# Performance work log

Hardware: AMD Instinct MI355X
Metric: run time of the kernel (lower is better)

## Reference

```python
import jax, jax.numpy as jnp
import numpy as np

I, H, O = 32, 64, 8  # input_size, hidden_layer, output_size
B, T = 4096, 256


def setup_inputs() -> dict:
    key = jax.random.key(0)
    ks = jax.random.split(key, 7)
    s_ih = 1.0 / np.sqrt(H)
    return {
        "x": jax.random.normal(ks[0], (B, T, I), dtype=jnp.float32),
        # PyTorch nn.LSTM params, gate order [i, f, g, o]
        "W_ih": jax.random.uniform(ks[1], (4 * H, I), jnp.float32, -s_ih, s_ih),
        "W_hh": jax.random.uniform(ks[2], (4 * H, H), jnp.float32, -s_ih, s_ih),
        "b_ih": jax.random.uniform(ks[3], (4 * H,), jnp.float32, -s_ih, s_ih),
        "b_hh": jax.random.uniform(ks[4], (4 * H,), jnp.float32, -s_ih, s_ih),
        "W_fc": jax.random.uniform(ks[5], (O, H), jnp.float32, -s_ih, s_ih),
        "b_fc": jax.random.uniform(ks[6], (O,), jnp.float32, -s_ih, s_ih),
    }


def reference(x, W_ih, W_hh, b_ih, b_hh, W_fc, b_fc):
    # Precompute input-to-hidden projections for all timesteps in one GEMM.
    # [B, T, 4H]
    x_proj = jnp.einsum('bti,gi->btg', x, W_ih) + b_ih + b_hh

    def step(carry, xp_t):
        h, c = carry  # [B, H] each
        gates = xp_t + h @ W_hh.T  # [B, 4H]
        i_g, f_g, g_g, o_g = jnp.split(gates, 4, axis=-1)
        i_g = jax.nn.sigmoid(i_g)
        f_g = jax.nn.sigmoid(f_g)
        g_g = jnp.tanh(g_g)
        o_g = jax.nn.sigmoid(o_g)
        c = f_g * c + i_g * g_g
        h = o_g * jnp.tanh(c)
        return (h, c), None

    h0 = jnp.zeros((x.shape[0], H), dtype=x.dtype)
    c0 = jnp.zeros((x.shape[0], H), dtype=x.dtype)
    # scan over time axis: move T to leading axis
    (h_T, c_T), _ = jax.lax.scan(step, (h0, c0), jnp.swapaxes(x_proj, 0, 1))
    # out[:, -1, :] == final hidden state for single-layer batch_first LSTM
    return h_T @ W_fc.T + b_fc
```

## Files before the change

### kernel.cpp

```cpp
#include <hip/hip_runtime.h>
#include <hip/hip_bf16.h>


#define T_LEN 256
#define I_SZ  32
#define H_SZ  64
#define O_SZ  8
#define BR    8
#define HS    72

typedef __attribute__((ext_vector_type(8))) short short8;
typedef __attribute__((ext_vector_type(4))) float f32x4;
typedef __attribute__((ext_vector_type(2))) float f32x2;

static __device__ __forceinline__ unsigned fbits(float f) {
    union { float f; unsigned u; } v; v.f = f; return v.u;
}
static __device__ __forceinline__ unsigned pk2t(float lo, float hi) {
    return __builtin_amdgcn_perm(fbits(hi), fbits(lo), 0x07060302u);
}
static __device__ __forceinline__ short f2bf_rne(float f) {
    union { __hip_bfloat16 b; short s; } u;
    u.b = __float2bfloat16(f);
    return u.s;
}
static __device__ __forceinline__ f32x2 rcp2(f32x2 d) {
    f32x2 r;
    r.x = __builtin_amdgcn_rcpf(d.x);
    r.y = __builtin_amdgcn_rcpf(d.y);
    return r;
}
static __device__ __forceinline__ f32x2 fma2(f32x2 a, f32x2 b, f32x2 c) {
    return __builtin_elementwise_fma(a, b, c);
}
static __device__ __forceinline__ f32x2 tanh2(f32x2 x) {
    f32x2 x2 = x * x;
    f32x2 n  = fma2(x2 + 105.0f, x2, (f32x2)(945.0f));
    f32x2 d  = fma2(fma2((f32x2)(15.0f), x2, (f32x2)(420.0f)), x2, (f32x2)(945.0f));
    f32x2 r  = (x * n) * rcp2(d);
    r = __builtin_elementwise_min(r, (f32x2)(1.0f));
    r = __builtin_elementwise_max(r, (f32x2)(-1.0f));
    return r;
}
static __device__ __forceinline__ f32x2 sig2(f32x2 x) {
    f32x2 x2 = x * x;
    f32x2 n  = fma2(x2 + 420.0f, x2, (f32x2)(15120.0f));
    f32x2 d  = fma2(fma2((f32x2)(60.0f), x2, (f32x2)(6720.0f)), x2, (f32x2)(60480.0f));
    f32x2 r  = fma2(x * n, rcp2(d), (f32x2)(0.5f));
    r = __builtin_elementwise_min(r, (f32x2)(1.0f));
    r = __builtin_elementwise_max(r, (f32x2)(0.0f));
    return r;
}

__global__ __launch_bounds__(256, 2)
void lstm_fused_kernel(const float* __restrict__ x,
                       const float* __restrict__ W_ih,
                       const float* __restrict__ W_hh,
                       const float* __restrict__ b_ih,
                       const float* __restrict__ b_hh,
                       const float* __restrict__ W_fc,
                       const float* __restrict__ b_fc,
                       float* __restrict__ out)
{
    __shared__ short hbuf[2][8][HS];
    __shared__ float Hf[BR][64];

    const int tid  = threadIdx.x;
    const int wave = tid >> 6;
    const int lane = tid & 63;
    const int quad = lane >> 4;
    const int nlow = lane & 15;
    const int jw   = wave * 16 + nlow;
    const int b0   = blockIdx.x * BR;

    const int fr = (nlow < 8) ? nlow : (((nlow & 4) ? 6 : 2) + (nlow & 1));
    const int ra = ((quad & 1) << 2) | (quad & 2);

    short8 bfrag[4][3];
    f32x4  biasf[4];
    for (int g = 0; g < 4; ++g) {
        const int col = g * 64 + jw;
        {
            const float* wr = W_ih + col * I_SZ + quad * 8;
            short8 f;
            #pragma unroll
            for (int e = 0; e < 8; ++e) f[e] = f2bf_rne(wr[e]);
            bfrag[g][0] = f;
        }
        #pragma unroll
        for (int kt = 1; kt < 3; ++kt) {
            const float* wr = W_hh + col * H_SZ + (kt - 1) * 32 + quad * 8;
            short8 f;
            #pragma unroll
            for (int e = 0; e < 8; ++e) f[e] = f2bf_rne(wr[e]);
            bfrag[g][kt] = f;
        }
        const float bg = b_ih[col] + b_hh[col];
        biasf[g] = (f32x4){bg, bg, bg, bg};
    }

    for (int q = tid; q < 2 * 8 * HS; q += 256) ((short*)hbuf)[q] = (short)0;

    const float* xb = x + ((size_t)(b0 + fr) * T_LEN) * I_SZ + quad * 8;

    float4 nx[16];
    short8 sc[8];
    #pragma unroll
    for (int s = 0; s < 8; ++s) {
        nx[2*s]   = *(const float4*)(xb + s * I_SZ);
        nx[2*s+1] = *(const float4*)(xb + s * I_SZ + 4);
    }
    #pragma unroll
    for (int s = 0; s < 8; ++s) {
        union { uint4 u; short8 v; } w;
        w.u.x = pk2t(nx[2*s].x,   nx[2*s].y);
        w.u.y = pk2t(nx[2*s].z,   nx[2*s].w);
        w.u.z = pk2t(nx[2*s+1].x, nx[2*s+1].y);
        w.u.w = pk2t(nx[2*s+1].z, nx[2*s+1].w);
        sc[s] = w.v;
    }

    const short* rb[2] = { &hbuf[0][fr][quad * 8], &hbuf[1][fr][quad * 8] };
    short*       wb[2] = { &hbuf[0][ra][jw],       &hbuf[1][ra][jw] };

    f32x2 cc = {0.f, 0.f};
    f32x2 hh = {0.f, 0.f};

    for (int ch = 0; ch < 32; ++ch) {
        #pragma unroll
        for (int tc = 0; tc < 8; ++tc) {
            const int t = ch * 8 + tc;

            __syncthreads();

            const short* hr = rb[t & 1];
            short8 a1 = *(const short8*)(hr);
            short8 a2 = *(const short8*)(hr + 32);

            if (tc == 0 && ch + 1 < 32) {
                const float* nxt = xb + (t + 8) * I_SZ;
                #pragma unroll
                for (int s = 0; s < 8; ++s) {
                    nx[2*s]   = *(const float4*)(nxt + s * I_SZ);
                    nx[2*s+1] = *(const float4*)(nxt + s * I_SZ + 4);
                }
            }

            const short8 ax = sc[tc];

            f32x4 acc[4];
            #pragma unroll
            for (int g = 0; g < 4; ++g) {
                f32x4 a = __builtin_amdgcn_mfma_f32_16x16x32_bf16(ax, bfrag[g][0], biasf[g], 0, 0, 0);
                a = __builtin_amdgcn_mfma_f32_16x16x32_bf16(a1, bfrag[g][1], a, 0, 0, 0);
                a = __builtin_amdgcn_mfma_f32_16x16x32_bf16(a2, bfrag[g][2], a, 0, 0, 0);
                acc[g] = a;
            }

            if (tc == 7 && ch + 1 < 32) {
                #pragma unroll
                for (int s = 0; s < 8; ++s) {
                    union { uint4 u; short8 v; } w;
                    w.u.x = pk2t(nx[2*s].x,   nx[2*s].y);
                    w.u.y = pk2t(nx[2*s].z,   nx[2*s].w);
                    w.u.z = pk2t(nx[2*s+1].x, nx[2*s+1].y);
                    w.u.w = pk2t(nx[2*s+1].z, nx[2*s+1].w);
                    sc[s] = w.v;
                }
            }

            f32x2 pI = {acc[0][0], acc[0][1]};
            f32x2 pF = {acc[1][0], acc[1][1]};
            f32x2 pG = {acc[2][0], acc[2][1]};
            f32x2 pO = {acc[3][0], acc[3][1]};

            f32x2 iv = sig2(pI);
            f32x2 fv = sig2(pF);
            f32x2 gv = tanh2(pG);
            f32x2 ov = sig2(pO);
            cc = fma2(fv, cc, iv * gv);
            hh = ov * tanh2(cc);

            short* hw = wb[(t + 1) & 1];
            hw[0]  = (short)((fbits(hh.x) + 0x8000u) >> 16);
            hw[HS] = (short)((fbits(hh.y) + 0x8000u) >> 16);
        }
    }

    Hf[ra][jw]     = hh.x;
    Hf[ra + 1][jw] = hh.y;
    __syncthreads();

    if (tid < BR * O_SZ) {
        const int r = tid >> 3;
        const int o = tid & 7;
        const float* wf = W_fc + o * H_SZ;
        float acc = b_fc[o];
        #pragma unroll
        for (int jx = 0; jx < H_SZ; ++jx) acc += Hf[r][jx] * wf[jx];
        out[(size_t)(b0 + r) * O_SZ + o] = acc;
    }
}

extern "C" void kernel_launch(void* const* d_in, const int* in_sizes, int n_in,
                              void* d_out, int out_size, void* d_ws, size_t ws_size,
                              hipStream_t stream) {
    const float* x    = (const float*)d_in[0];
    const float* W_ih = (const float*)d_in[1];
    const float* W_hh = (const float*)d_in[2];
    const float* b_ih = (const float*)d_in[3];
    const float* b_hh = (const float*)d_in[4];
    const float* W_fc = (const float*)d_in[5];
    const float* b_fc = (const float*)d_in[6];
    float* out = (float*)d_out;

    const int B = 4096;
    lstm_fused_kernel<<<dim3(B / BR), dim3(256), 0, stream>>>(
        x, W_ih, W_hh, b_ih, b_hh, W_fc, b_fc, out);
}
```

Measured before the change: 314.7 us.

## Process 16 batch rows per block to fill all MFMA rows

Raises rows per block from 8 to 16 so every row of the 16x16 MFMA tile carries a real batch row, instead of the earlier duplicated-row mapping that used only half the output. Each lane now runs the gate nonlinearities on 4 values rather than 2, and clamping uses fmed3. The grid shrinks to 256 blocks and launch bounds drop to one block per CU. The intent is to halve the number of serial recurrence steps per unit of batch work, at the cost of more per-thread activation math and fewer blocks to hide latency.

```diff
diff --git a/kernel.cpp b/kernel.cpp
--- a/kernel.cpp
+++ b/kernel.cpp
@@ -6,12 +6,11 @@
 #define I_SZ  32
 #define H_SZ  64
 #define O_SZ  8
-#define BR    8
+#define BR    16
 #define HS    72
 
 typedef __attribute__((ext_vector_type(8))) short short8;
 typedef __attribute__((ext_vector_type(4))) float f32x4;
-typedef __attribute__((ext_vector_type(2))) float f32x2;
 
 static __device__ __forceinline__ unsigned fbits(float f) {
     union { float f; unsigned u; } v; v.f = f; return v.u;
@@ -24,35 +23,41 @@
     u.b = __float2bfloat16(f);
     return u.s;
 }
-static __device__ __forceinline__ f32x2 rcp2(f32x2 d) {
-    f32x2 r;
+static __device__ __forceinline__ f32x4 rcp4(f32x4 d) {
+    f32x4 r;
     r.x = __builtin_amdgcn_rcpf(d.x);
     r.y = __builtin_amdgcn_rcpf(d.y);
+    r.z = __builtin_amdgcn_rcpf(d.z);
+    r.w = __builtin_amdgcn_rcpf(d.w);
     return r;
 }
-static __device__ __forceinline__ f32x2 fma2(f32x2 a, f32x2 b, f32x2 c) {
+static __device__ __forceinline__ f32x4 fma4(f32x4 a, f32x4 b, f32x4 c) {
     return __builtin_elementwise_fma(a, b, c);
 }
-static __device__ __forceinline__ f32x2 tanh2(f32x2 x) {
-    f32x2 x2 = x * x;
-    f32x2 n  = fma2(x2 + 105.0f, x2, (f32x2)(945.0f));
-    f32x2 d  = fma2(fma2((f32x2)(15.0f), x2, (f32x2)(420.0f)), x2, (f32x2)(945.0f));
-    f32x2 r  = (x * n) * rcp2(d);
-    r = __builtin_elementwise_min(r, (f32x2)(1.0f));
-    r = __builtin_elementwise_max(r, (f32x2)(-1.0f));
+static __device__ __forceinline__ f32x4 clamp4(f32x4 x, float lo, float hi) {
+    f32x4 r;
+    r.x = __builtin_amdgcn_fmed3f(x.x, lo, hi);
+    r.y = __builtin_amdgcn_fmed3f(x.y, lo, hi);
+    r.z = __builtin_amdgcn_fmed3f(x.z, lo, hi);
+    r.w = __builtin_amdgcn_fmed3f(x.w, lo, hi);
     return r;
 }
-static __device__ __forceinline__ f32x2 sig2(f32x2 x) {
-    f32x2 x2 = x * x;
-    f32x2 n  = fma2(x2 + 420.0f, x2, (f32x2)(15120.0f));
-    f32x2 d  = fma2(fma2((f32x2)(60.0f), x2, (f32x2)(6720.0f)), x2, (f32x2)(60480.0f));
-    f32x2 r  = fma2(x * n, rcp2(d), (f32x2)(0.5f));
-    r = __builtin_elementwise_min(r, (f32x2)(1.0f));
-    r = __builtin_elementwise_max(r, (f32x2)(0.0f));
-    return r;
-}
-
-__global__ __launch_bounds__(256, 2)
+static __device__ __forceinline__ f32x4 tanh4(f32x4 x) {
+    f32x4 x2 = x * x;
+    f32x4 n  = fma4(x2 + 105.0f, x2, (f32x4)(945.0f));
+    f32x4 d  = fma4(fma4((f32x4)(15.0f), x2, (f32x4)(420.0f)), x2, (f32x4)(945.0f));
+    f32x4 r  = (x * n) * rcp4(d);
+    return clamp4(r, -1.0f, 1.0f);
+}
+static __device__ __forceinline__ f32x4 sig4(f32x4 x) {
+    f32x4 x2 = x * x;
+    f32x4 n  = fma4(x2 + 420.0f, x2, (f32x4)(15120.0f));
+    f32x4 d  = fma4(fma4((f32x4)(60.0f), x2, (f32x4)(6720.0f)), x2, (f32x4)(60480.0f));
+    f32x4 r  = fma4(x * n, rcp4(d), (f32x4)(0.5f));
+    return clamp4(r, 0.0f, 1.0f);
+}
+
+__global__ __launch_bounds__(256, 1)
 void lstm_fused_kernel(const float* __restrict__ x,
                        const float* __restrict__ W_ih,
                        const float* __restrict__ W_hh,
@@ -62,19 +67,17 @@
                        const float* __restrict__ b_fc,
                        float* __restrict__ out)
 {
-    __shared__ short hbuf[2][8][HS];
+    __shared__ short hbuf[2][BR][HS];
     __shared__ float Hf[BR][64];
 
-    const int tid  = threadIdx.x;
-    const int wave = tid >> 6;
-    const int lane = tid & 63;
-    const int quad = lane >> 4;
-    const int nlow = lane & 15;
-    const int jw   = wave * 16 + nlow;
-    const int b0   = blockIdx.x * BR;
-
-    const int fr = (nlow < 8) ? nlow : (((nlow & 4) ? 6 : 2) + (nlow & 1));
-    const int ra = ((quad & 1) << 2) | (quad & 2);
+    const int tid   = threadIdx.x;
+    const int wave  = tid >> 6;
+    const int lane  = tid & 63;
+    const int quad  = lane >> 4;
+    const int nlow  = lane & 15;
+    const int jw    = wave * 16 + nlow;
+    const int rbase = quad * 4;
+    const int b0    = blockIdx.x * BR;
 
     short8 bfrag[4][3];
     f32x4  biasf[4];
@@ -99,9 +102,9 @@
         biasf[g] = (f32x4){bg, bg, bg, bg};
     }
 
-    for (int q = tid; q < 2 * 8 * HS; q += 256) ((short*)hbuf)[q] = (short)0;
-
-    const float* xb = x + ((size_t)(b0 + fr) * T_LEN) * I_SZ + quad * 8;
+    for (int q = tid; q < 2 * BR * HS; q += 256) ((short*)hbuf)[q] = (short)0;
+
+    const float* xb = x + ((size_t)(b0 + nlow) * T_LEN) * I_SZ + quad * 8;
 
     float4 nx[16];
     short8 sc[8];
@@ -120,11 +123,11 @@
         sc[s] = w.v;
     }
 
-    const short* rb[2] = { &hbuf[0][fr][quad * 8], &hbuf[1][fr][quad * 8] };
-    short*       wb[2] = { &hbuf[0][ra][jw],       &hbuf[1][ra][jw] };
-
-    f32x2 cc = {0.f, 0.f};
-    f32x2 hh = {0.f, 0.f};
+    const short* rb[2] = { &hbuf[0][nlow][quad * 8], &hbuf[1][nlow][quad * 8] };
+    short*       wb[2] = { &hbuf[0][rbase][jw],      &hbuf[1][rbase][jw] };
+
+    f32x4 cc = {0.f, 0.f, 0.f, 0.f};
+    f32x4 hh = {0.f, 0.f, 0.f, 0.f};
 
     for (int ch = 0; ch < 32; ++ch) {
         #pragma unroll
@@ -169,26 +172,25 @@
                 }
             }
 
-            f32x2 pI = {acc[0][0], acc[0][1]};
-            f32x2 pF = {acc[1][0], acc[1][1]};
-            f32x2 pG = {acc[2][0], acc[2][1]};
-            f32x2 pO = {acc[3][0], acc[3][1]};
-
-            f32x2 iv = sig2(pI);
-            f32x2 fv = sig2(pF);
-            f32x2 gv = tanh2(pG);
-            f32x2 ov = sig2(pO);
-            cc = fma2(fv, cc, iv * gv);
-            hh = ov * tanh2(cc);
+            f32x4 iv = sig4(acc[0]);
+            f32x4 fv = sig4(acc[1]);
+            f32x4 gv = tanh4(acc[2]);
+            f32x4 ov = sig4(acc[3]);
+            cc = fma4(fv, cc, iv * gv);
+            hh = ov * tanh4(cc);
 
             short* hw = wb[(t + 1) & 1];
-            hw[0]  = (short)((fbits(hh.x) + 0x8000u) >> 16);
-            hw[HS] = (short)((fbits(hh.y) + 0x8000u) >> 16);
+            hw[0 * HS] = (short)((fbits(hh.x) + 0x8000u) >> 16);
+            hw[1 * HS] = (short)((fbits(hh.y) + 0x8000u) >> 16);
+            hw[2 * HS] = (short)((fbits(hh.z) + 0x8000u) >> 16);
+            hw[3 * HS] = (short)((fbits(hh.w) + 0x8000u) >> 16);
         }
     }
 
-    Hf[ra][jw]     = hh.x;
-    Hf[ra + 1][jw] = hh.y;
+    Hf[rbase + 0][jw] = hh.x;
+    Hf[rbase + 1][jw] = hh.y;
+    Hf[rbase + 2][jw] = hh.z;
+    Hf[rbase + 3][jw] = hh.w;
     __syncthreads();
 
     if (tid < BR * O_SZ) {
```

New measurement: 305.7 us. 2.9% less time.
